# Optimization experiments

Measured on AMD Instinct MI355X. Metric: run time of the kernel, lower is better.

Reference implementation:

```python
import jax, jax.numpy as jnp
import numpy as np

T_VALUES = (4.0, 16.0, 64.0, 256.0)
EPS = 1e-05


def setup_inputs() -> dict:
    key = jax.random.key(0)
    k1, = jax.random.split(key, 1)
    B, F, T = 32, 128, 2000
    x = jax.random.uniform(k1, (B, F, T), dtype=jnp.float32)
    # learned log-parameters, initialized exactly like the torch module
    log_alpha = jnp.full((F,), jnp.log(0.8), dtype=jnp.float32)
    log_delta = jnp.full((F,), jnp.log(10.0), dtype=jnp.float32)
    log_r = jnp.full((F,), jnp.log(0.25), dtype=jnp.float32)
    return {"x": x, "log_alpha": log_alpha, "log_delta": log_delta, "log_r": log_r}


def _mrpcen(x, log_alpha, log_delta, log_r):
    # x: (B, F, T)
    t = jnp.asarray(T_VALUES, dtype=x.dtype)                      # (n_t,)
    s = (jnp.sqrt(1.0 + 4.0 * t ** 2) - 1.0) / (2.0 * t ** 2)     # (n_t,)
    s = s[:, None, None]                                          # (n_t,1,1)

    n_t = len(T_VALUES)
    B, F, T = x.shape
    xt = jnp.moveaxis(x, -1, 0)                                   # (T, B, F)
    m0 = jnp.broadcast_to(xt[0], (n_t, B, F))                     # (n_t, B, F)

    def step(m, x_frame):
        m_new = (1.0 - s) * m + s * x_frame                        # (n_t,B,F)
        return m_new, m_new

    _, ms = jax.lax.scan(step, m0, xt[1:])                        # (T-1, n_t, B, F)
    M = jnp.concatenate([m0[None], ms], axis=0)                   # (T, n_t, B, F)
    M = jnp.moveaxis(M, 0, -1)                                    # (n_t, B, F, T)

    alpha = jnp.exp(log_alpha)[:, None]                           # (F,1)
    delta = jnp.exp(log_delta)[:, None]                           # (F,1)
    r = jnp.exp(log_r)[:, None]                                   # (F,1)

    eps = jnp.asarray(EPS, dtype=x.dtype)
    smooth = jnp.exp(-alpha * (jnp.log(eps) + jnp.log1p(M / eps)))  # (n_t,B,F,T)
    pcen = (x[None] * smooth + delta) ** r - delta ** r             # (n_t,B,F,T)
    return jnp.transpose(pcen, (1, 0, 2, 3))                        # (B,n_t,F,T)


def reference(x, log_alpha, log_delta, log_r):
    return _mrpcen(x, log_alpha, log_delta, log_r)
```

## Files before the change

### kernel.cpp

```cpp
#include <hip/hip_runtime.h>
#include <math.h>


#define NT      4
#define TLEN    2000
#define FDIM    128
#define CHUNK   32
#define LSTRIDE 33
#define ROWPAD  (64 * LSTRIDE)
#define WPB     4

__global__ __launch_bounds__(256) void mrpcen_kernel(
    const float* __restrict__ x,
    const float* __restrict__ log_alpha,
    const float* __restrict__ log_delta,
    const float* __restrict__ log_r,
    float* __restrict__ out,
    int rows)
{
    __shared__ float stage[WPB][ROWPAD];

    const int w    = threadIdx.x >> 6;
    const int lane = threadIdx.x & 63;
    const int row  = blockIdx.x * WPB + w;
    const bool live = (row < rows);
    const int b = row >> 7;
    const int f = row & (FDIM - 1);

    if (live) {
        const float4* xg4 = (const float4*)(x + (size_t)row * TLEN);
        for (int q = lane; q < TLEN / 4; q += 64) {
            float4 v = xg4[q];
            int p0 = q * 4;
            int bi = (p0 >> 5) * LSTRIDE + (p0 & 31);
            stage[w][bi + 0] = v.x; stage[w][bi + 1] = v.y;
            stage[w][bi + 2] = v.z; stage[w][bi + 3] = v.w;
        }
    }
    __syncthreads();

    float xr[CHUNK];
#pragma unroll
    for (int j = 0; j < CHUNK; ++j)
        xr[j] = stage[w][lane * LSTRIDE + j];

    const int ff = live ? f : 0;
    const float alpha = __expf(log_alpha[ff]);
    const float delta = __expf(log_delta[ff]);
    const float rr    = __expf(log_r[ff]);
    const float dr    = __expf(rr * __logf(delta));
    const float eps   = 1e-5f;

    const float tvals[NT] = {4.f, 16.f, 64.f, 256.f};

#pragma unroll 1
    for (int ti = 0; ti < NT; ++ti) {
        const float t  = tvals[ti];
        const float s  = (sqrtf(1.f + 4.f * t * t) - 1.f) / (2.f * t * t);
        const float cs = 1.f - s;

        float c2  = cs * cs, c4 = c2 * c2, c8 = c4 * c4;
        float c16 = c8 * c8, c32 = c16 * c16;
        float A = (lane == 0) ? 0.f : (lane < 62) ? c32 : (lane == 62) ? c16 : 1.f;

        float B = 0.f;
#pragma unroll
        for (int j = 0; j < CHUNK; ++j) {
            int pos  = lane * CHUNK + j;
            float a  = (pos < TLEN) ? cs : 1.0f;
            float bb = (pos < TLEN) ? s * xr[j] : 0.0f;
            if (pos == 0) { a = 0.0f; bb = xr[j]; }
            B = fmaf(a, B, bb);
        }

#pragma unroll
        for (int off = 1; off < 64; off <<= 1) {
            float Ap = __shfl_up(A, off, 64);
            float Bp = __shfl_up(B, off, 64);
            if (lane >= off) {
                B = fmaf(A, Bp, B);
                A = A * Ap;
            }
        }
        float m = __shfl_up(B, 1, 64);

#pragma unroll
        for (int j = 0; j < CHUNK; ++j) {
            int pos  = lane * CHUNK + j;
            float a  = (pos < TLEN) ? cs : 1.0f;
            float bb = (pos < TLEN) ? s * xr[j] : 0.0f;
            if (pos == 0) { a = 0.0f; bb = xr[j]; }
            m = fmaf(a, m, bb);
            if (pos < TLEN) {
                float smooth = __expf(-alpha * __logf(eps + m));
                float v      = fmaf(xr[j], smooth, delta);
                stage[w][lane * LSTRIDE + j] = __expf(rr * __logf(v)) - dr;
            }
        }
        __syncthreads();

        if (live) {
            float* gout = out + ((size_t)(b * NT + ti) * FDIM + f) * TLEN;
            for (int pos = lane; pos < TLEN; pos += 64) {
                int idx = (pos >> 5) * LSTRIDE + (pos & 31);
                gout[pos] = stage[w][idx];
            }
        }
        __syncthreads();
    }
}

extern "C" void kernel_launch(void* const* d_in, const int* in_sizes, int n_in,
                              void* d_out, int out_size, void* d_ws, size_t ws_size,
                              hipStream_t stream) {
    const float* x  = (const float*)d_in[0];
    const float* la = (const float*)d_in[1];
    const float* ld = (const float*)d_in[2];
    const float* lr = (const float*)d_in[3];
    float* out = (float*)d_out;

    const int rows   = in_sizes[0] / TLEN;
    const int blocks = (rows + WPB - 1) / WPB;
    hipLaunchKernelGGL(mrpcen_kernel, dim3(blocks), dim3(256), 0, stream,
                       x, la, ld, lr, out, rows);
}
```

Before: 177.4 us.

## Drop LDS staging; load and store rows directly with per-lane float4 accesses

Removes the shared-memory staging buffer and block barriers. Each lane now loads its contiguous 32-element chunk with float4 global reads and writes its outputs directly as float4 stores, instead of transposing through LDS for coalesced access. It also swaps __expf/__logf for exp2f/log2f and lets dead warps exit early. The risk is that accesses become strided across lanes (each lane 128 bytes apart), which may lower coalescing efficiency compared to the earlier lane-contiguous stores.

Result: slower. 196.0 us (+10.5%).

```diff
diff --git a/kernel.cpp b/kernel.cpp
--- a/kernel.cpp
+++ b/kernel.cpp
@@ -1,14 +1,11 @@
 #include <hip/hip_runtime.h>
-#include <math.h>
 
 
-#define NT      4
-#define TLEN    2000
-#define FDIM    128
-#define CHUNK   32
-#define LSTRIDE 33
-#define ROWPAD  (64 * LSTRIDE)
-#define WPB     4
+#define NT    4
+#define TLEN  2000
+#define FDIM  128
+#define CHUNK 32
+#define WPB   4
 
 __global__ __launch_bounds__(256) void mrpcen_kernel(
     const float* __restrict__ x,
@@ -18,38 +15,31 @@
     float* __restrict__ out,
     int rows)
 {
-    __shared__ float stage[WPB][ROWPAD];
-
     const int w    = threadIdx.x >> 6;
     const int lane = threadIdx.x & 63;
     const int row  = blockIdx.x * WPB + w;
-    const bool live = (row < rows);
+    if (row >= rows) return;
     const int b = row >> 7;
     const int f = row & (FDIM - 1);
 
-    if (live) {
-        const float4* xg4 = (const float4*)(x + (size_t)row * TLEN);
-        for (int q = lane; q < TLEN / 4; q += 64) {
-            float4 v = xg4[q];
-            int p0 = q * 4;
-            int bi = (p0 >> 5) * LSTRIDE + (p0 & 31);
-            stage[w][bi + 0] = v.x; stage[w][bi + 1] = v.y;
-            stage[w][bi + 2] = v.z; stage[w][bi + 3] = v.w;
-        }
+    float xr[CHUNK];
+    const float* xrow = x + (size_t)row * TLEN;
+    const int base = lane * CHUNK;
+#pragma unroll
+    for (int q = 0; q < CHUNK / 4; ++q) {
+        int pos = base + q * 4;
+        float4 v = (pos < TLEN) ? ((const float4*)xrow)[pos >> 2]
+                                : make_float4(0.f, 0.f, 0.f, 0.f);
+        xr[q * 4 + 0] = v.x; xr[q * 4 + 1] = v.y;
+        xr[q * 4 + 2] = v.z; xr[q * 4 + 3] = v.w;
     }
-    __syncthreads();
 
-    float xr[CHUNK];
-#pragma unroll
-    for (int j = 0; j < CHUNK; ++j)
-        xr[j] = stage[w][lane * LSTRIDE + j];
-
-    const int ff = live ? f : 0;
-    const float alpha = __expf(log_alpha[ff]);
-    const float delta = __expf(log_delta[ff]);
-    const float rr    = __expf(log_r[ff]);
-    const float dr    = __expf(rr * __logf(delta));
+    const float alpha = __expf(log_alpha[f]);
+    const float delta = __expf(log_delta[f]);
+    const float rr    = __expf(log_r[f]);
+    const float dr    = exp2f(rr * log2f(delta));
     const float eps   = 1e-5f;
+    const float nalpha = -alpha;
 
     const float tvals[NT] = {4.f, 16.f, 64.f, 256.f};
 
@@ -66,7 +56,7 @@
         float B = 0.f;
 #pragma unroll
         for (int j = 0; j < CHUNK; ++j) {
-            int pos  = lane * CHUNK + j;
+            int pos  = base + j;
             float a  = (pos < TLEN) ? cs : 1.0f;
             float bb = (pos < TLEN) ? s * xr[j] : 0.0f;
             if (pos == 0) { a = 0.0f; bb = xr[j]; }
@@ -84,29 +74,25 @@
         }
         float m = __shfl_up(B, 1, 64);
 
+        float* gout = out + ((size_t)(b * NT + ti) * FDIM + f) * TLEN;
+        float o4[4];
 #pragma unroll
         for (int j = 0; j < CHUNK; ++j) {
-            int pos  = lane * CHUNK + j;
+            int pos  = base + j;
             float a  = (pos < TLEN) ? cs : 1.0f;
             float bb = (pos < TLEN) ? s * xr[j] : 0.0f;
             if (pos == 0) { a = 0.0f; bb = xr[j]; }
             m = fmaf(a, m, bb);
-            if (pos < TLEN) {
-                float smooth = __expf(-alpha * __logf(eps + m));
-                float v      = fmaf(xr[j], smooth, delta);
-                stage[w][lane * LSTRIDE + j] = __expf(rr * __logf(v)) - dr;
+            float smooth = exp2f(nalpha * log2f(eps + m));
+            float v      = fmaf(xr[j], smooth, delta);
+            o4[j & 3]    = exp2f(rr * log2f(v)) - dr;
+            if ((j & 3) == 3) {
+                int p0 = base + (j & ~3);
+                if (p0 < TLEN)
+                    ((float4*)gout)[p0 >> 2] =
+                        make_float4(o4[0], o4[1], o4[2], o4[3]);
             }
         }
-        __syncthreads();
-
-        if (live) {
-            float* gout = out + ((size_t)(b * NT + ti) * FDIM + f) * TLEN;
-            for (int pos = lane; pos < TLEN; pos += 64) {
-                int idx = (pos >> 5) * LSTRIDE + (pos & 31);
-                gout[pos] = stage[w][idx];
-            }
-        }
-        __syncthreads();
     }
 }
 
```
